# Optimization experiments

Hardware: AMD Instinct MI355X
Metric: run time of the kernel (lower is better)

## Reference

```python
import jax, jax.numpy as jnp
import numpy as np

B, S, H, NH = 2, 2048, 1024, 16
HD = H // NH  # head_dim = 64


def setup_inputs() -> dict:
    key = jax.random.key(0)
    k1, k2, k3, k4, k5 = jax.random.split(key, 5)
    hidden_states = jax.random.normal(k1, (B, S, H), dtype=jnp.float32)
    # additive causal mask: 0 on/below diagonal, -1e9 above
    causal = jnp.tril(jnp.ones((S, S), dtype=jnp.bool_))
    attention_mask = jnp.where(causal, 0.0, -1e9).astype(jnp.float32)[None, None, :, :]
    scale = 0.02
    Wq = jax.random.normal(k2, (H, H), dtype=jnp.float32) * scale
    Wk = jax.random.normal(k3, (H, H), dtype=jnp.float32) * scale
    Wv = jax.random.normal(k4, (H, H), dtype=jnp.float32) * scale
    Wo = jax.random.normal(k5, (H, H), dtype=jnp.float32) * scale
    return {"hidden_states": hidden_states, "attention_mask": attention_mask,
            "Wq": Wq, "Wk": Wk, "Wv": Wv, "Wo": Wo}


def reference(hidden_states, attention_mask, Wq, Wk, Wv, Wo):
    b, s, _ = hidden_states.shape
    # nn.Linear: y = x @ W.T
    q = (hidden_states @ Wq.T).reshape(b, s, NH, HD).transpose(0, 2, 1, 3)  # [B,NH,S,HD]
    k = (hidden_states @ Wk.T).reshape(b, s, NH, HD).transpose(0, 2, 1, 3)
    v = (hidden_states @ Wv.T).reshape(b, s, NH, HD).transpose(0, 2, 1, 3)
    scores = jnp.einsum('bhqd,bhkd->bhqk', q, k) / jnp.sqrt(jnp.float32(HD))
    scores = scores + attention_mask
    attn = jax.nn.softmax(scores, axis=-1)
    out = jnp.einsum('bhqk,bhkd->bhqd', attn, v)  # [B,NH,S,HD]
    out = out.transpose(0, 2, 1, 3).reshape(b, s, H)
    return out @ Wo.T
```

## Files before the change

kernel.cpp:

```cpp
#include <hip/hip_runtime.h>
#include <hip/hip_bf16.h>

#define B_   2
#define S_   2048
#define H_   1024
#define NH_  16
#define HD_  64
#define MTOT 4096
#define KD   1024

typedef __attribute__((ext_vector_type(4)))  float    f32x4;
typedef __attribute__((ext_vector_type(16))) float    f32x16;
typedef __attribute__((ext_vector_type(8)))  short    bf16x8;
typedef __attribute__((ext_vector_type(2)))  unsigned u32x2;
typedef __attribute__((ext_vector_type(4)))  unsigned u32x4;

__device__ inline short f2bf(float x) {
    union { float f; unsigned u; } v; v.f = x;
    unsigned r = v.u + 0x7fffu + ((v.u >> 16) & 1u);
    return (short)(r >> 16);
}
__device__ inline unsigned pk2(float lo, float hi) {
    return (unsigned)(unsigned short)f2bf(lo) | ((unsigned)(unsigned short)f2bf(hi) << 16);
}
__device__ inline unsigned cvtpk(float lo, float hi) {
    unsigned r;
    asm("v_cvt_pk_bf16_f32 %0, %1, %2" : "=v"(r) : "v"(lo), "v"(hi));
    return r;
}
__device__ inline void gload16(const void* g, void* l) {
    __builtin_amdgcn_global_load_lds(
        (const __attribute__((address_space(1))) unsigned*)g,
        (__attribute__((address_space(3))) unsigned*)l, 16, 0, 0);
}

__global__ __launch_bounds__(256) void cvt_x(const float* __restrict__ x,
                                             unsigned* __restrict__ xb) {
    const size_t i = ((size_t)blockIdx.x * 256 + threadIdx.x) * 8;
    const f32x4 a = *(const f32x4*)(x + i);
    const f32x4 b = *(const f32x4*)(x + i + 4);
    u32x4 p;
    p[0] = pk2(a[0], a[1]); p[1] = pk2(a[2], a[3]);
    p[2] = pk2(b[0], b[1]); p[3] = pk2(b[2], b[3]);
    *(u32x4*)(xb + i / 2) = p;
}

__global__ __launch_bounds__(256) void wcvt(const float* __restrict__ W0,
                                            const float* __restrict__ W1,
                                            const float* __restrict__ W2,
                                            const float* __restrict__ W3,
                                            unsigned* __restrict__ wb) {
    const float* W = (blockIdx.y == 0) ? W0 : (blockIdx.y == 1) ? W1
                   : (blockIdx.y == 2) ? W2 : W3;
    const size_t i = ((size_t)blockIdx.x * 256 + threadIdx.x) * 8;
    const f32x4 a = *(const f32x4*)(W + i);
    const f32x4 b = *(const f32x4*)(W + i + 4);
    u32x4 p;
    p[0] = pk2(a[0], a[1]); p[1] = pk2(a[2], a[3]);
    p[2] = pk2(b[0], b[1]); p[3] = pk2(b[2], b[3]);
    *(u32x4*)(wb + (size_t)blockIdx.y * (H_ * KD / 2) + i / 2) = p;
}

template <int MODE>
__global__ __launch_bounds__(256) void gemm_m97(const short* __restrict__ A,
                                                const short* __restrict__ Wb,
                                                short* __restrict__ outb,
                                                float* __restrict__ outf) {
    __shared__ short Sm[128 * 128];
    short* As = Sm;
    short* Bs = Sm + 8192;

    const int tid = threadIdx.x, wave = tid >> 6, lane = tid & 63;
    const int wm = (wave >> 1) * 64, wn = (wave & 1) * 64;
    const int m0 = blockIdx.x * 128;

    int n0, widx;
    if constexpr (MODE == 0) {
        widx = blockIdx.y >> 3;
        n0 = (blockIdx.y & 7) * 128;
    } else {
        widx = 0;
        n0 = blockIdx.y * 128;
    }
    const short* W = Wb + (size_t)widx * H_ * KD;

    f32x4 acc[4][4] = {};

    for (int k0 = 0; k0 < KD; k0 += 64) {
#pragma unroll
        for (int c = 0; c < 4; ++c) {
            const int lin = wave * 4096 + c * 1024 + lane * 16;
            const int row = lin >> 7;
            const int col = (lin & 127) ^ ((row & 7) << 4);
            gload16(A + (size_t)(m0 + row) * KD + k0 + (col >> 1),
                    (char*)As + wave * 4096 + c * 1024);
            gload16(W + (size_t)(n0 + row) * KD + k0 + (col >> 1),
                    (char*)Bs + wave * 4096 + c * 1024);
        }
        __syncthreads();

#pragma unroll
        for (int ks = 0; ks < 2; ++ks) {
            bf16x8 af[4], bf[4];
#pragma unroll
            for (int i = 0; i < 4; ++i) {
                const int row = wm + i * 16 + (lane & 15);
                af[i] = *(const bf16x8*)((char*)As + row * 128 +
                        ((ks * 64 + (lane >> 4) * 16) ^ ((row & 7) << 4)));
            }
#pragma unroll
            for (int j = 0; j < 4; ++j) {
                const int row = wn + j * 16 + (lane & 15);
                bf[j] = *(const bf16x8*)((char*)Bs + row * 128 +
                        ((ks * 64 + (lane >> 4) * 16) ^ ((row & 7) << 4)));
            }
#pragma unroll
            for (int i = 0; i < 4; ++i)
#pragma unroll
                for (int j = 0; j < 4; ++j)
                    acc[i][j] = __builtin_amdgcn_mfma_f32_16x16x32_bf16(af[i], bf[j], acc[i][j], 0, 0, 0);
        }
        __syncthreads();
    }

    if constexpr (MODE == 0) {
#pragma unroll
        for (int i = 0; i < 4; ++i)
#pragma unroll
            for (int j = 0; j < 4; ++j)
#pragma unroll
                for (int r = 0; r < 4; ++r) {
                    const int mi = wm + i * 16 + (lane >> 4) * 4 + r;
                    const int ni = wn + j * 16 + (lane & 15);
                    const int byt = (mi * 256 + ni * 2) ^ ((mi & 7) << 4);
                    *(short*)((char*)Sm + byt) = f2bf(acc[i][j][r]);
                }
        __syncthreads();
        const int row = tid >> 1, half = tid & 1;
        const int m = m0 + row, bb = m >> 11, s = m & 2047;
        const int hh = (n0 >> 6) + half;
        short* dst = outb + (size_t)widx * MTOT * H_ +
                     (((size_t)(bb * NH_ + hh)) * S_ + s) * HD_;
#pragma unroll
        for (int k = 0; k < 8; ++k) {
            const int byt = (row * 256 + half * 128 + k * 16) ^ ((row & 7) << 4);
            *(bf16x8*)(dst + k * 8) = *(const bf16x8*)((char*)Sm + byt);
        }
    } else {
#pragma unroll
        for (int i = 0; i < 4; ++i)
#pragma unroll
            for (int j = 0; j < 4; ++j)
#pragma unroll
                for (int r = 0; r < 4; ++r) {
                    const int m = m0 + wm + i * 16 + (lane >> 4) * 4 + r;
                    const int n = n0 + wn + j * 16 + (lane & 15);
                    outf[(size_t)m * H_ + n] = acc[i][j][r];
                }
    }
}

__global__ __launch_bounds__(256) void flash2(const short* __restrict__ Qb,
                                              const short* __restrict__ Kb,
                                              const short* __restrict__ Vb,
                                              short* __restrict__ Ob) {
    const int bx = blockIdx.x;
    const int hi = bx >> 8, u = bx & 255;
    const int h = u >> 4, tq = u & 15;
    const int qt = hi ? (15 - tq) : tq;
    const int b  = hi;

    const int tid = threadIdx.x, wave = tid >> 6, lane = tid & 63;
    const int q0 = qt * 128;
    const int qw0 = q0 + wave * 32;
    const size_t hoff = ((size_t)(b * NH_ + h)) * S_ * HD_;
    const short* Q = Qb + hoff;
    const short* K = Kb + hoff;
    const short* V = Vb + hoff;

    __shared__ short Ks[64 * 64];
    __shared__ short Vt[64 * 64];

    const int ql = lane & 31;
    const int hh = lane >> 5;

    bf16x8 qf[4];
#pragma unroll
    for (int ds = 0; ds < 4; ++ds)
        qf[ds] = *(const bf16x8*)(Q + (size_t)(qw0 + ql) * HD_ + ds * 16 + hh * 8);

    f32x16 ot[2] = {};
    float mrun = -1e30f, lrun = 0.f;
    const float c2 = 0.18033688011112042f;

    const int nkt = 2 * qt + 2;
    for (int kt = 0; kt < nkt; ++kt) {
        __syncthreads();
#pragma unroll
        for (int c = 0; c < 2; ++c) {
            const int lin = wave * 2048 + c * 1024 + lane * 16;
            const int row = lin >> 7;
            const int col = (lin & 127) ^ ((row & 7) << 4);
            gload16(K + (size_t)(kt * 64 + row) * HD_ + (col >> 1),
                    (char*)Ks + wave * 2048 + c * 1024);
        }
        {
            const int kk = (tid & 31) * 2, d0 = (tid >> 5) * 8;
            const bf16x8 v0 = *(const bf16x8*)(V + (size_t)(kt * 64 + kk) * HD_ + d0);
            const bf16x8 v1 = *(const bf16x8*)(V + (size_t)(kt * 64 + kk + 1) * HD_ + d0);
#pragma unroll
            for (int i = 0; i < 8; ++i) {
                const int d = d0 + i;
                const int byt = d * 128 + kk * 2;
                *(unsigned*)((char*)Vt + (byt ^ ((d & 7) << 4))) =
                    (unsigned)(unsigned short)v0[i] | ((unsigned)(unsigned short)v1[i] << 16);
            }
        }
        __syncthreads();

        if (kt * 64 <= qw0 + 31) {
            const bool need_mask = (kt * 64 + 63) > qw0;

            f32x16 st[2] = {};
#pragma unroll
            for (int t = 0; t < 2; ++t)
#pragma unroll
                for (int ds = 0; ds < 4; ++ds) {
                    const int row = t * 32 + ql;
                    const bf16x8 kf = *(const bf16x8*)((char*)Ks + row * 128 +
                            ((ds * 32 + hh * 16) ^ ((row & 7) << 4)));
                    st[t] = __builtin_amdgcn_mfma_f32_32x32x16_bf16(kf, qf[ds], st[t], 0, 0, 0);
                }

            float sraw[32];
#pragma unroll
            for (int t = 0; t < 2; ++t)
#pragma unroll
                for (int r = 0; r < 16; ++r) {
                    float v = st[t][r];
                    if (need_mask) {
                        const int key = kt * 64 + t * 32 + (r & 3) + 8 * (r >> 2) + 4 * hh;
                        if (key > qw0 + ql) v = -1e30f;
                    }
                    sraw[t * 16 + r] = v;
                }

            float tr[16];
#pragma unroll
            for (int i = 0; i < 16; ++i) tr[i] = fmaxf(sraw[i], sraw[i + 16]);
#pragma unroll
            for (int stp = 8; stp >= 1; stp >>= 1)
#pragma unroll
                for (int i = 0; i < 8; ++i)
                    if (i < stp) tr[i] = fmaxf(tr[i], tr[i + stp]);
            const float pmax = fmaxf(tr[0], __shfl_xor(tr[0], 32, 64));

            if (!__all((pmax - mrun) <= 44.36f)) {
                const float mnew = fmaxf(mrun, pmax);
                const float corr = exp2f((mrun - mnew) * c2);
                mrun = mnew;
                lrun *= corr;
#pragma unroll
                for (int dt = 0; dt < 2; ++dt)
#pragma unroll
                    for (int r = 0; r < 16; ++r) ot[dt][r] *= corr;
            }
            const float mc = mrun * c2;

            float p[32];
#pragma unroll
            for (int i = 0; i < 32; ++i) p[i] = exp2f(fmaf(sraw[i], c2, -mc));
            float ts[16];
#pragma unroll
            for (int i = 0; i < 16; ++i) ts[i] = p[i] + p[i + 16];
#pragma unroll
            for (int stp = 8; stp >= 1; stp >>= 1)
#pragma unroll
                for (int i = 0; i < 8; ++i)
                    if (i < stp) ts[i] += ts[i + stp];
            lrun += ts[0] + __shfl_xor(ts[0], 32, 64);

#pragma unroll
            for (int ks = 0; ks < 4; ++ks) {
                const int t = ks >> 1, rb = (ks & 1) * 8;
                const unsigned a0 = cvtpk(p[t * 16 + rb + 0], p[t * 16 + rb + 1]);
                const unsigned a1 = cvtpk(p[t * 16 + rb + 2], p[t * 16 + rb + 3]);
                const unsigned a2 = cvtpk(p[t * 16 + rb + 4], p[t * 16 + rb + 5]);
                const unsigned a3 = cvtpk(p[t * 16 + rb + 6], p[t * 16 + rb + 7]);
                const unsigned s0 = __shfl_xor(a0, 32, 64);
                const unsigned s1 = __shfl_xor(a1, 32, 64);
                const unsigned s2 = __shfl_xor(a2, 32, 64);
                const unsigned s3 = __shfl_xor(a3, 32, 64);
                u32x4 pw;
                pw[0] = hh ? s2 : a0;
                pw[1] = hh ? s3 : a1;
                pw[2] = hh ? a2 : s0;
                pw[3] = hh ? a3 : s1;
                const bf16x8 pf = __builtin_bit_cast(bf16x8, pw);
#pragma unroll
                for (int dt = 0; dt < 2; ++dt) {
                    const int row = dt * 32 + ql;
                    const bf16x8 vf = *(const bf16x8*)((char*)Vt + row * 128 +
                            ((ks * 32 + hh * 16) ^ ((row & 7) << 4)));
                    ot[dt] = __builtin_amdgcn_mfma_f32_32x32x16_bf16(vf, pf, ot[dt], 0, 0, 0);
                }
            }
        }
    }

    const float inv = 1.f / lrun;
    short* orow = Ob + ((size_t)(b * S_) + q0 + wave * 32 + ql) * H_ + h * HD_;
#pragma unroll
    for (int dt = 0; dt < 2; ++dt)
#pragma unroll
        for (int g4 = 0; g4 < 4; ++g4) {
            const int dbase = dt * 32 + 8 * g4 + 4 * hh;
            u32x2 w;
            w[0] = cvtpk(ot[dt][g4 * 4 + 0] * inv, ot[dt][g4 * 4 + 1] * inv);
            w[1] = cvtpk(ot[dt][g4 * 4 + 2] * inv, ot[dt][g4 * 4 + 3] * inv);
            *(u32x2*)(orow + dbase) = w;
        }
}

extern "C" void kernel_launch(void* const* d_in, const int* in_sizes, int n_in,
                              void* d_out, int out_size, void* d_ws, size_t ws_size,
                              hipStream_t stream) {
    const float* x  = (const float*)d_in[0];
    const float* Wq = (const float*)d_in[2];
    const float* Wk = (const float*)d_in[3];
    const float* Wv = (const float*)d_in[4];
    const float* Wo = (const float*)d_in[5];
    float* out = (float*)d_out;

    short* qkv = (short*)d_ws;
    short* xb  = qkv + (size_t)3 * MTOT * H_;
    short* wb  = xb + (size_t)MTOT * H_;

    cvt_x<<<2048, 256, 0, stream>>>(x, (unsigned*)xb);
    wcvt<<<dim3(512, 4), 256, 0, stream>>>(Wq, Wk, Wv, Wo, (unsigned*)wb);

    gemm_m97<0><<<dim3(32, 24), 256, 0, stream>>>(xb, wb, qkv, nullptr);

    flash2<<<dim3(512), 256, 0, stream>>>(
        qkv, qkv + (size_t)MTOT * H_, qkv + (size_t)2 * MTOT * H_, xb);

    gemm_m97<1><<<dim3(32, 8), 256, 0, stream>>>(
        xb, wb + (size_t)3 * H_ * KD, nullptr, out);
}
```

Before: 150.5 us.

## Double-buffer K/V tiles in flash attention and prefetch the next tile during compute

Splits the K and transposed-V shared-memory tiles into two buffers. The next tile's K is issued via async global-to-LDS loads and its V is loaded into registers before computing on the current tile, so load latency overlaps the MFMA and softmax work and one barrier per iteration goes away. It also replaces the tree max reduction with v_max3 chains and raises wave priority around the MFMA blocks. This doubles LDS use, may lower occupancy, and adds register pressure from holding V in registers across the compute.

New measurement: 152.0 us. Within noise of the previous version (+1.0%).

```diff
diff --git a/kernel.cpp b/kernel.cpp
--- a/kernel.cpp
+++ b/kernel.cpp
@@ -26,6 +26,11 @@
 __device__ inline unsigned cvtpk(float lo, float hi) {
     unsigned r;
     asm("v_cvt_pk_bf16_f32 %0, %1, %2" : "=v"(r) : "v"(lo), "v"(hi));
+    return r;
+}
+__device__ inline float max3f(float a, float b, float c) {
+    float r;
+    asm("v_max3_f32 %0, %1, %2, %3" : "=v"(r) : "v"(a), "v"(b), "v"(c));
     return r;
 }
 __device__ inline void gload16(const void* g, void* l) {
@@ -178,8 +183,8 @@
     const short* K = Kb + hoff;
     const short* V = Vb + hoff;
 
-    __shared__ short Ks[64 * 64];
-    __shared__ short Vt[64 * 64];
+    __shared__ short Ks[2][64 * 64];
+    __shared__ short Vt[2][64 * 64];
 
     const int ql = lane & 31;
     const int hh = lane >> 5;
@@ -193,44 +198,59 @@
     float mrun = -1e30f, lrun = 0.f;
     const float c2 = 0.18033688011112042f;
 
-    const int nkt = 2 * qt + 2;
-    for (int kt = 0; kt < nkt; ++kt) {
-        __syncthreads();
+    const int kk = (tid & 31) * 2, d0v = (tid >> 5) * 8;
+    bf16x8 vr0, vr1;
+    auto stageK = [&](int kt, int buf) {
 #pragma unroll
         for (int c = 0; c < 2; ++c) {
             const int lin = wave * 2048 + c * 1024 + lane * 16;
             const int row = lin >> 7;
             const int col = (lin & 127) ^ ((row & 7) << 4);
             gload16(K + (size_t)(kt * 64 + row) * HD_ + (col >> 1),
-                    (char*)Ks + wave * 2048 + c * 1024);
-        }
-        {
-            const int kk = (tid & 31) * 2, d0 = (tid >> 5) * 8;
-            const bf16x8 v0 = *(const bf16x8*)(V + (size_t)(kt * 64 + kk) * HD_ + d0);
-            const bf16x8 v1 = *(const bf16x8*)(V + (size_t)(kt * 64 + kk + 1) * HD_ + d0);
-#pragma unroll
-            for (int i = 0; i < 8; ++i) {
-                const int d = d0 + i;
-                const int byt = d * 128 + kk * 2;
-                *(unsigned*)((char*)Vt + (byt ^ ((d & 7) << 4))) =
-                    (unsigned)(unsigned short)v0[i] | ((unsigned)(unsigned short)v1[i] << 16);
-            }
-        }
-        __syncthreads();
+                    (char*)Ks[buf] + wave * 2048 + c * 1024);
+        }
+    };
+    auto loadV = [&](int kt) {
+        vr0 = *(const bf16x8*)(V + (size_t)(kt * 64 + kk) * HD_ + d0v);
+        vr1 = *(const bf16x8*)(V + (size_t)(kt * 64 + kk + 1) * HD_ + d0v);
+    };
+    auto writeV = [&](int buf) {
+#pragma unroll
+        for (int i = 0; i < 8; ++i) {
+            const int d = d0v + i;
+            const int byt = d * 128 + kk * 2;
+            *(unsigned*)((char*)Vt[buf] + (byt ^ ((d & 7) << 4))) =
+                (unsigned)(unsigned short)vr0[i] | ((unsigned)(unsigned short)vr1[i] << 16);
+        }
+    };
+
+    const int nkt = 2 * qt + 2;
+
+    stageK(0, 0);
+    loadV(0);
+    writeV(0);
+    __syncthreads();
+
+    int cur = 0;
+    for (int kt = 0; kt < nkt; ++kt) {
+        const bool pre = (kt + 1 < nkt);
+        if (pre) { stageK(kt + 1, cur ^ 1); loadV(kt + 1); }
 
         if (kt * 64 <= qw0 + 31) {
             const bool need_mask = (kt * 64 + 63) > qw0;
 
             f32x16 st[2] = {};
+            __builtin_amdgcn_s_setprio(1);
 #pragma unroll
             for (int t = 0; t < 2; ++t)
 #pragma unroll
                 for (int ds = 0; ds < 4; ++ds) {
                     const int row = t * 32 + ql;
-                    const bf16x8 kf = *(const bf16x8*)((char*)Ks + row * 128 +
+                    const bf16x8 kf = *(const bf16x8*)((char*)Ks[cur] + row * 128 +
                             ((ds * 32 + hh * 16) ^ ((row & 7) << 4)));
                     st[t] = __builtin_amdgcn_mfma_f32_32x32x16_bf16(kf, qf[ds], st[t], 0, 0, 0);
                 }
+            __builtin_amdgcn_s_setprio(0);
 
             float sraw[32];
 #pragma unroll
@@ -245,15 +265,14 @@
                     sraw[t * 16 + r] = v;
                 }
 
-            float tr[16];
-#pragma unroll
-            for (int i = 0; i < 16; ++i) tr[i] = fmaxf(sraw[i], sraw[i + 16]);
-#pragma unroll
-            for (int stp = 8; stp >= 1; stp >>= 1)
-#pragma unroll
-                for (int i = 0; i < 8; ++i)
-                    if (i < stp) tr[i] = fmaxf(tr[i], tr[i + stp]);
-            const float pmax = fmaxf(tr[0], __shfl_xor(tr[0], 32, 64));
+            float ma = fmaxf(sraw[0], sraw[1]);
+            float mb = fmaxf(sraw[2], sraw[3]);
+#pragma unroll
+            for (int i = 4; i < 32; i += 4) {
+                ma = max3f(ma, sraw[i],     sraw[i + 1]);
+                mb = max3f(mb, sraw[i + 2], sraw[i + 3]);
+            }
+            const float pmax = fmaxf(fmaxf(ma, mb), __shfl_xor(fmaxf(ma, mb), 32, 64));
 
             if (!__all((pmax - mrun) <= 44.36f)) {
                 const float mnew = fmaxf(mrun, pmax);
@@ -297,15 +316,21 @@
                 pw[2] = hh ? a2 : s0;
                 pw[3] = hh ? a3 : s1;
                 const bf16x8 pf = __builtin_bit_cast(bf16x8, pw);
+                __builtin_amdgcn_s_setprio(1);
 #pragma unroll
                 for (int dt = 0; dt < 2; ++dt) {
                     const int row = dt * 32 + ql;
-                    const bf16x8 vf = *(const bf16x8*)((char*)Vt + row * 128 +
+                    const bf16x8 vf = *(const bf16x8*)((char*)Vt[cur] + row * 128 +
                             ((ks * 32 + hh * 16) ^ ((row & 7) << 4)));
                     ot[dt] = __builtin_amdgcn_mfma_f32_32x32x16_bf16(vf, pf, ot[dt], 0, 0, 0);
                 }
-            }
-        }
+                __builtin_amdgcn_s_setprio(0);
+            }
+        }
+
+        if (pre) writeV(cur ^ 1);
+        __syncthreads();
+        cur ^= 1;
     }
 
     const float inv = 1.f / lrun;
```
